# Optimization experiments

Hardware: AMD Instinct MI355X
Metric: run time of the kernel (lower is better)

## Reference

```python
import jax, jax.numpy as jnp
import numpy as np

B, DIM, HW = 2, 2, 512
HID, OUT, NL = 64, 3, 4  # no_layers=4 -> NL+1 filters


def _linear2d(w, b, inp):
    # 1x1 conv: w [o,i], inp [b,i,x,y] -> [b,o,x,y]
    return jnp.einsum('oi,bixy->boxy', w, inp) + b[None, :, None, None]


def _gabor_filter(x, w, b, mu_l, gamma_l, theta_l):
    # Rotated gaussian window. x: [B,2,H,W]
    ang = 2.0 * jnp.pi * theta_l  # [C]
    c, s = jnp.cos(ang), jnp.sin(ang)
    # rotation_matrix: rows [[cos, sin], [-sin, cos]] per channel -> [C,2,2]
    R = jnp.stack([jnp.stack([c, s], -1), jnp.stack([-s, c], -1)], -2)
    diff = x[:, None] - mu_l[None, :, :, None, None]          # [B,C,2,H,W]
    rot = jnp.einsum('coi,bcixy->bcoxy', R, diff)              # [B,C,2,H,W]
    g = jnp.exp(-0.5 * jnp.sum((gamma_l[None, :, :, None, None] * rot) ** 2, axis=2))
    return g * jnp.sin(_linear2d(w, b, x))                     # [B,C,H,W]


def setup_inputs() -> dict:
    key = jax.random.key(0)
    ks = jax.random.split(key, 10)
    inv_sqrt_hid = 1.0 / np.sqrt(HID)
    return {
        'x': jax.random.uniform(ks[0], (B, DIM, HW, HW), jnp.float32, -1.0, 1.0),
        'filt_w': jax.random.normal(ks[1], (NL + 1, HID, DIM), jnp.float32) * 0.1,
        'filt_b': jax.random.uniform(ks[2], (NL + 1, HID), jnp.float32, -np.pi, np.pi),
        'mu': jax.random.uniform(ks[3], (NL + 1, HID, DIM), jnp.float32, -1.0, 1.0),
        'gamma': jax.random.uniform(ks[4], (NL + 1, HID, DIM), jnp.float32, 0.5, 6.0),
        'theta': jax.random.uniform(ks[5], (NL + 1, HID), jnp.float32),
        'lin_w': jax.random.uniform(ks[6], (NL, HID, HID), jnp.float32, -inv_sqrt_hid, inv_sqrt_hid),
        'lin_b': jax.random.normal(ks[7], (NL, HID), jnp.float32) * 0.01,
        'out_w': jax.random.normal(ks[8], (OUT, HID), jnp.float32) * inv_sqrt_hid,
        'out_b': jax.random.normal(ks[9], (OUT,), jnp.float32) * 0.01,
    }


def reference(x, filt_w, filt_b, mu, gamma, theta, lin_w, lin_b, out_w, out_b):
    out = _gabor_filter(x, filt_w[0], filt_b[0], mu[0], gamma[0], theta[0])
    for i in range(1, NL + 1):
        lin = _linear2d(lin_w[i - 1], lin_b[i - 1], out)
        out = _gabor_filter(x, filt_w[i], filt_b[i], mu[i], gamma[i], theta[i]) * lin
    return _linear2d(out_w, out_b, out)  # [B,OUT,H,W]
```

## Files before the change

### kernel.cpp

```cpp
#include <hip/hip_runtime.h>
#include <hip/hip_bf16.h>
#include <math.h>

#define HW2 262144
#define TWO_PI     6.28318530717958647693f
#define INV_TWO_PI 0.15915494309189533577f
#define LOG2E      1.44269504088896340736f

typedef float  f32x4  __attribute__((ext_vector_type(4)));
typedef float  f32x8  __attribute__((ext_vector_type(8)));
typedef short  s16x8  __attribute__((ext_vector_type(8)));
typedef short  s16x4  __attribute__((ext_vector_type(4)));
typedef unsigned short ushort_t;

template <int I> struct ic { static constexpr int v = I; };
template <int I, int N, typename F>
__device__ __forceinline__ void sfor(F&& f) {
    if constexpr (I < N) { f(ic<I>{}); sfor<I + 1, N>(f); }
}

__device__ __forceinline__ ushort_t bf16_hi(float v) {
    __hip_bfloat16 h = __float2bfloat16(v);
    return __builtin_bit_cast(ushort_t, h);
}
__device__ __forceinline__ float bf16_tof(ushort_t u) {
    unsigned int x = ((unsigned int)u) << 16;
    return __builtin_bit_cast(float, x);
}

#define WS_WHI  15360
#define WS_WLO  48128
#define WS_WOH  80896
#define WS_WOL  82944

__global__ void gabor_pre(const float* __restrict__ filt_w,
                          const float* __restrict__ filt_b,
                          const float* __restrict__ mu,
                          const float* __restrict__ gamma,
                          const float* __restrict__ theta,
                          const float* __restrict__ lin_w,
                          const float* __restrict__ out_w,
                          float* __restrict__ pcq,
                          ushort_t* __restrict__ whi, ushort_t* __restrict__ wlo,
                          ushort_t* __restrict__ wouthi, ushort_t* __restrict__ woutlo) {
    int t = blockIdx.x * 256 + threadIdx.x;
    if (t < 320) {
        int i = t;
        float ang = TWO_PI * theta[i];
        float cs = cosf(ang), sn = sinf(ang);
        float g0 = gamma[i*2+0], g1 = gamma[i*2+1];
        float g0s = g0*g0, g1s = g1*g1;
        float cs2 = cs*cs, sn2 = sn*sn;
        float A = -0.5f * LOG2E * (g0s*cs2 + g1s*sn2);
        float B = -LOG2E * (cs*sn*(g0s - g1s));
        float C = -0.5f * LOG2E * (g0s*sn2 + g1s*cs2);
        float m0 = mu[i*2+0], m1 = mu[i*2+1];
        float* o = pcq + i*12;
        o[0] = A;  o[1] = B;  o[2] = C;
        o[3] = -(2.0f*A*m0 + B*m1);
        o[4] = -(B*m0 + 2.0f*C*m1);
        o[5] = A*m0*m0 + B*m0*m1 + C*m1*m1;
        o[6] = filt_w[i*2+0] * INV_TWO_PI;
        o[7] = filt_w[i*2+1] * INV_TWO_PI;
        o[8] = filt_b[i] * INV_TWO_PI;
        o[9] = 0.0f; o[10] = 0.0f; o[11] = 0.0f;
    } else if (t < 320 + 16384) {
        int i = t - 320;
        float w = lin_w[i];
        ushort_t h = bf16_hi(w);
        whi[i] = h;
        wlo[i] = bf16_hi(w - bf16_tof(h));
    } else if (t < 320 + 16384 + 1024) {
        int i = t - (320 + 16384);
        int m = i >> 6;
        float w = (m < 3) ? out_w[i] : 0.0f;
        ushort_t h = bf16_hi(w);
        wouthi[i] = h;
        woutlo[i] = bf16_hi(w - bf16_tof(h));
    }
}

__device__ __forceinline__ float geval(f32x4 qa, f32x4 qb, float br,
                                       float x0, float x1,
                                       float x02, float x11, float x12) {
    float t = fmaf(qa[0], x02, fmaf(qa[1], x11,
              fmaf(qa[2], x12, fmaf(qa[3], x0, fmaf(qb[0], x1, qb[1])))));
    float e  = __builtin_amdgcn_exp2f(t);
    float sa = fmaf(qb[2], x0, fmaf(qb[3], x1, br));
    return e * __builtin_amdgcn_sinf(sa);
}

__global__ __launch_bounds__(128, 2) void gabor_mfma(
    const float* __restrict__ x, const float* __restrict__ lin_b,
    const float* __restrict__ out_b, const float* __restrict__ pcq,
    const ushort_t* __restrict__ whi, const ushort_t* __restrict__ wlo,
    const ushort_t* __restrict__ wouthi, const ushort_t* __restrict__ woutlo,
    float* __restrict__ out) {
    __shared__ __attribute__((aligned(16))) unsigned char hbuf2[2][16384];
    const int lane = threadIdx.x & 63;
    const int wid  = threadIdx.x >> 6;
    const int g    = lane >> 4;
    const int lm   = lane & 15;
    const int base = blockIdx.x * 128 + wid * 64;
    unsigned char* hbuf = hbuf2[wid];

    f32x4 x0v, x1v, x02v, x11v, x12v;
    int pixo[4];
    sfor<0, 4>([&](auto NI) {
        int P  = base + NI.v*16 + lm;
        int bb = P >> 18, pix = P & (HW2 - 1);
        const float* xb = x + bb*(2*HW2) + pix;
        float a = xb[0], b = xb[HW2];
        x0v[NI.v] = a;  x1v[NI.v] = b;
        x02v[NI.v] = a*a;  x11v[NI.v] = a*b;  x12v[NI.v] = b*b;
        pixo[NI.v] = bb*(3*HW2) + pix;
    });

    sfor<0, 2>([&](auto KC) {
        f32x8 vv[4];
        sfor<0, 8>([&](auto J) {
            const float* q = pcq + (KC.v*32 + g*8 + J.v)*12;
            f32x4 qa = *(const f32x4*)q, qb = *(const f32x4*)(q + 4);
            float br = q[8];
            sfor<0, 4>([&](auto NI) {
                vv[NI.v][J.v] = geval(qa, qb, br, x0v[NI.v], x1v[NI.v],
                                      x02v[NI.v], x11v[NI.v], x12v[NI.v]);
            });
        });
        sfor<0, 4>([&](auto NI) {
            s16x8 fh, fl;
            sfor<0, 8>([&](auto J) {
                float v = vv[NI.v][J.v];
                ushort_t h = bf16_hi(v);
                fh[J.v] = (short)h;
                fl[J.v] = (short)bf16_hi(v - bf16_tof(h));
            });
            int px  = NI.v*16 + lm;
            int blk = (4*KC.v + g) ^ (px & 7);
            char* p0 = (char*)hbuf + px*128 + blk*16;
            *(s16x8*)(p0)        = fh;
            *(s16x8*)(p0 + 8192) = fl;
        });
    });

#pragma unroll 1
    for (int l = 1; l <= 4; ++l) {
        __syncthreads();
        const ushort_t* whl = whi + (l-1)*4096;
        const ushort_t* wll = wlo + (l-1)*4096;
        const float*    bv  = lin_b + (l-1)*64;
        f32x4 acc[4][4];
        sfor<0, 4>([&](auto MI) {
            f32x4 bias = *(const f32x4*)(bv + MI.v*16 + 4*g);
            sfor<0, 4>([&](auto NI) { acc[MI.v][NI.v] = bias; });
        });
        sfor<0, 2>([&](auto KC) {
            s16x8 bh[4], bl[4];
            sfor<0, 4>([&](auto NI) {
                int px  = NI.v*16 + lm;
                int blk = (4*KC.v + g) ^ (px & 7);
                const char* p0 = (const char*)hbuf + px*128 + blk*16;
                bh[NI.v] = *(const s16x8*)(p0);
                bl[NI.v] = *(const s16x8*)(p0 + 8192);
            });
            sfor<0, 4>([&](auto MI) {
                int off = (MI.v*16 + lm)*64 + KC.v*32 + g*8;
                s16x8 ah = *(const s16x8*)(whl + off);
                s16x8 al = *(const s16x8*)(wll + off);
                sfor<0, 4>([&](auto NI) {
                    f32x4 a = acc[MI.v][NI.v];
                    a = __builtin_amdgcn_mfma_f32_16x16x32_bf16(ah, bh[NI.v], a, 0, 0, 0);
                    a = __builtin_amdgcn_mfma_f32_16x16x32_bf16(ah, bl[NI.v], a, 0, 0, 0);
                    a = __builtin_amdgcn_mfma_f32_16x16x32_bf16(al, bh[NI.v], a, 0, 0, 0);
                    acc[MI.v][NI.v] = a;
                });
            });
        });
        __syncthreads();
        const float* pcl = pcq + l*768;
        sfor<0, 4>([&](auto MI) {
            f32x4 vo[4];
            sfor<0, 4>([&](auto R) {
                const float* q = pcl + (MI.v*16 + 4*g + R.v)*12;
                f32x4 qa = *(const f32x4*)q, qb = *(const f32x4*)(q + 4);
                float br = q[8];
                sfor<0, 4>([&](auto NI) {
                    vo[NI.v][R.v] = geval(qa, qb, br, x0v[NI.v], x1v[NI.v],
                                          x02v[NI.v], x11v[NI.v], x12v[NI.v])
                                    * acc[MI.v][NI.v][R.v];
                });
            });
            sfor<0, 4>([&](auto NI) {
                s16x4 fh, fl;
                sfor<0, 4>([&](auto R) {
                    float v = vo[NI.v][R.v];
                    ushort_t h = bf16_hi(v);
                    fh[R.v] = (short)h;
                    fl[R.v] = (short)bf16_hi(v - bf16_tof(h));
                });
                int px  = NI.v*16 + lm;
                int blk = (2*MI.v + (g >> 1)) ^ (px & 7);
                char* p0 = (char*)hbuf + px*128 + blk*16 + (g & 1)*8;
                *(s16x4*)(p0)        = fh;
                *(s16x4*)(p0 + 8192) = fl;
            });
        });
    }

    __syncthreads();
    f32x4 ao[4];
    sfor<0, 4>([&](auto NI) { ao[NI.v] = (f32x4)(0.0f); });
    sfor<0, 2>([&](auto KC) {
        s16x8 bh[4], bl[4];
        sfor<0, 4>([&](auto NI) {
            int px  = NI.v*16 + lm;
            int blk = (4*KC.v + g) ^ (px & 7);
            const char* p0 = (const char*)hbuf + px*128 + blk*16;
            bh[NI.v] = *(const s16x8*)(p0);
            bl[NI.v] = *(const s16x8*)(p0 + 8192);
        });
        int off = lm*64 + KC.v*32 + g*8;
        s16x8 ah = *(const s16x8*)(wouthi + off);
        s16x8 al = *(const s16x8*)(woutlo + off);
        sfor<0, 4>([&](auto NI) {
            f32x4 a = ao[NI.v];
            a = __builtin_amdgcn_mfma_f32_16x16x32_bf16(ah, bh[NI.v], a, 0, 0, 0);
            a = __builtin_amdgcn_mfma_f32_16x16x32_bf16(ah, bl[NI.v], a, 0, 0, 0);
            a = __builtin_amdgcn_mfma_f32_16x16x32_bf16(al, bh[NI.v], a, 0, 0, 0);
            ao[NI.v] = a;
        });
    });
    if (lane < 16) {
        float ob0 = out_b[0], ob1 = out_b[1], ob2 = out_b[2];
        sfor<0, 4>([&](auto NI) {
            float* po = out + pixo[NI.v];
            po[0]     = ao[NI.v][0] + ob0;
            po[HW2]   = ao[NI.v][1] + ob1;
            po[2*HW2] = ao[NI.v][2] + ob2;
        });
    }
}

extern "C" void kernel_launch(void* const* d_in, const int* in_sizes, int n_in,
                              void* d_out, int out_size, void* d_ws, size_t ws_size,
                              hipStream_t stream) {
    const float* x      = (const float*)d_in[0];
    const float* filt_w = (const float*)d_in[1];
    const float* filt_b = (const float*)d_in[2];
    const float* mu     = (const float*)d_in[3];
    const float* gamma  = (const float*)d_in[4];
    const float* theta  = (const float*)d_in[5];
    const float* lin_w  = (const float*)d_in[6];
    const float* lin_b  = (const float*)d_in[7];
    const float* out_w  = (const float*)d_in[8];
    const float* out_b  = (const float*)d_in[9];

    char* ws = (char*)d_ws;
    float*    pcq    = (float*)ws;
    ushort_t* whi    = (ushort_t*)(ws + WS_WHI);
    ushort_t* wlo    = (ushort_t*)(ws + WS_WLO);
    ushort_t* wouthi = (ushort_t*)(ws + WS_WOH);
    ushort_t* woutlo = (ushort_t*)(ws + WS_WOL);

    gabor_pre<<<70, 256, 0, stream>>>(filt_w, filt_b, mu, gamma, theta,
                                      lin_w, out_w, pcq, whi, wlo, wouthi, woutlo);
    gabor_mfma<<<4096, 128, 0, stream>>>(x, lin_b, out_b, pcq, whi, wlo,
                                         wouthi, woutlo, (float*)d_out);
}
```

Baseline: 158.2 us.

## Keep MFMA activations in registers via permuted K layout, dropping LDS round-trips

The lin and out weight columns are permuted in the preprocess kernel so that each MFMA accumulator output maps directly onto the B-operand fragment layout of the next layer. Activations can then stay in registers between layers, which removes the shared-memory staging buffer, the swizzled LDS stores and loads, and all __syncthreads. Block size goes from 128 to 256 threads with launch bounds (256,3). The cost is more live registers per thread (the bh/bl fragments for all pixel tiles), which may limit occupancy.

```diff
diff --git a/kernel.cpp b/kernel.cpp
--- a/kernel.cpp
+++ b/kernel.cpp
@@ -8,9 +8,7 @@
 #define LOG2E      1.44269504088896340736f
 
 typedef float  f32x4  __attribute__((ext_vector_type(4)));
-typedef float  f32x8  __attribute__((ext_vector_type(8)));
 typedef short  s16x8  __attribute__((ext_vector_type(8)));
-typedef short  s16x4  __attribute__((ext_vector_type(4)));
 typedef unsigned short ushort_t;
 
 template <int I> struct ic { static constexpr int v = I; };
@@ -26,6 +24,11 @@
 __device__ __forceinline__ float bf16_tof(ushort_t u) {
     unsigned int x = ((unsigned int)u) << 16;
     return __builtin_bit_cast(float, x);
+}
+
+__device__ __forceinline__ int kperm(int ks) {
+    int KC = ks >> 5, g = (ks >> 3) & 3, j = ks & 7;
+    return KC * 32 + (j >> 2) * 16 + g * 4 + (j & 3);
 }
 
 #define WS_WHI  15360
@@ -65,15 +68,16 @@
         o[8] = filt_b[i] * INV_TWO_PI;
         o[9] = 0.0f; o[10] = 0.0f; o[11] = 0.0f;
     } else if (t < 320 + 16384) {
-        int i = t - 320;
-        float w = lin_w[i];
+        int i  = t - 320;
+        int ks = i & 63;
+        float w = lin_w[(i - ks) + kperm(ks)];
         ushort_t h = bf16_hi(w);
         whi[i] = h;
         wlo[i] = bf16_hi(w - bf16_tof(h));
     } else if (t < 320 + 16384 + 1024) {
-        int i = t - (320 + 16384);
-        int m = i >> 6;
-        float w = (m < 3) ? out_w[i] : 0.0f;
+        int i  = t - (320 + 16384);
+        int m  = i >> 6, ks = i & 63;
+        float w = (m < 3) ? out_w[m*64 + kperm(ks)] : 0.0f;
         ushort_t h = bf16_hi(w);
         wouthi[i] = h;
         woutlo[i] = bf16_hi(w - bf16_tof(h));
@@ -90,19 +94,17 @@
     return e * __builtin_amdgcn_sinf(sa);
 }
 
-__global__ __launch_bounds__(128, 2) void gabor_mfma(
+__global__ __launch_bounds__(256, 3) void gabor_mfma(
     const float* __restrict__ x, const float* __restrict__ lin_b,
     const float* __restrict__ out_b, const float* __restrict__ pcq,
     const ushort_t* __restrict__ whi, const ushort_t* __restrict__ wlo,
     const ushort_t* __restrict__ wouthi, const ushort_t* __restrict__ woutlo,
     float* __restrict__ out) {
-    __shared__ __attribute__((aligned(16))) unsigned char hbuf2[2][16384];
     const int lane = threadIdx.x & 63;
     const int wid  = threadIdx.x >> 6;
     const int g    = lane >> 4;
     const int lm   = lane & 15;
-    const int base = blockIdx.x * 128 + wid * 64;
-    unsigned char* hbuf = hbuf2[wid];
+    const int base = blockIdx.x * 256 + wid * 64;
 
     f32x4 x0v, x1v, x02v, x11v, x12v;
     int pixo[4];
@@ -116,129 +118,91 @@
         pixo[NI.v] = bb*(3*HW2) + pix;
     });
 
-    sfor<0, 2>([&](auto KC) {
-        f32x8 vv[4];
-        sfor<0, 8>([&](auto J) {
-            const float* q = pcq + (KC.v*32 + g*8 + J.v)*12;
-            f32x4 qa = *(const f32x4*)q, qb = *(const f32x4*)(q + 4);
-            float br = q[8];
-            sfor<0, 4>([&](auto NI) {
-                vv[NI.v][J.v] = geval(qa, qb, br, x0v[NI.v], x1v[NI.v],
-                                      x02v[NI.v], x11v[NI.v], x12v[NI.v]);
-            });
-        });
-        sfor<0, 4>([&](auto NI) {
-            s16x8 fh, fl;
-            sfor<0, 8>([&](auto J) {
-                float v = vv[NI.v][J.v];
-                ushort_t h = bf16_hi(v);
-                fh[J.v] = (short)h;
-                fl[J.v] = (short)bf16_hi(v - bf16_tof(h));
-            });
-            int px  = NI.v*16 + lm;
-            int blk = (4*KC.v + g) ^ (px & 7);
-            char* p0 = (char*)hbuf + px*128 + blk*16;
-            *(s16x8*)(p0)        = fh;
-            *(s16x8*)(p0 + 8192) = fl;
-        });
+    s16x8 bh[4][2], bl[4][2];
+
+    auto mkfrag = [&](f32x4 vA, f32x4 vB, s16x8& fh, s16x8& fl) {
+        sfor<0, 4>([&](auto R) {
+            ushort_t hA = bf16_hi(vA[R.v]);
+            ushort_t hB = bf16_hi(vB[R.v]);
+            fh[R.v]     = (short)hA;
+            fh[R.v + 4] = (short)hB;
+            fl[R.v]     = (short)bf16_hi(vA[R.v] - bf16_tof(hA));
+            fl[R.v + 4] = (short)bf16_hi(vB[R.v] - bf16_tof(hB));
+        });
+    };
+
+    sfor<0, 4>([&](auto NI) {
+        f32x4 v[4];
+        sfor<0, 4>([&](auto MI) {
+            sfor<0, 4>([&](auto R) {
+                const float* q = pcq + (MI.v*16 + 4*g + R.v)*12;
+                f32x4 qa = *(const f32x4*)q, qb = *(const f32x4*)(q + 4);
+                v[MI.v][R.v] = geval(qa, qb, q[8], x0v[NI.v], x1v[NI.v],
+                                     x02v[NI.v], x11v[NI.v], x12v[NI.v]);
+            });
+        });
+        mkfrag(v[0], v[1], bh[NI.v][0], bl[NI.v][0]);
+        mkfrag(v[2], v[3], bh[NI.v][1], bl[NI.v][1]);
     });
 
 #pragma unroll 1
     for (int l = 1; l <= 4; ++l) {
-        __syncthreads();
         const ushort_t* whl = whi + (l-1)*4096;
         const ushort_t* wll = wlo + (l-1)*4096;
         const float*    bv  = lin_b + (l-1)*64;
-        f32x4 acc[4][4];
-        sfor<0, 4>([&](auto MI) {
-            f32x4 bias = *(const f32x4*)(bv + MI.v*16 + 4*g);
-            sfor<0, 4>([&](auto NI) { acc[MI.v][NI.v] = bias; });
-        });
+        const float*    pcl = pcq + l*768;
+        sfor<0, 4>([&](auto NI) {
+            constexpr int ni = NI.v;
+            f32x4 acc[4];
+            sfor<0, 4>([&](auto MI) {
+                acc[MI.v] = *(const f32x4*)(bv + MI.v*16 + 4*g);
+            });
+            sfor<0, 2>([&](auto KC) {
+                sfor<0, 4>([&](auto MI) {
+                    int off = (MI.v*16 + lm)*64 + KC.v*32 + g*8;
+                    s16x8 ah = *(const s16x8*)(whl + off);
+                    s16x8 al = *(const s16x8*)(wll + off);
+                    f32x4 a = acc[MI.v];
+                    a = __builtin_amdgcn_mfma_f32_16x16x32_bf16(ah, bh[ni][KC.v], a, 0, 0, 0);
+                    a = __builtin_amdgcn_mfma_f32_16x16x32_bf16(ah, bl[ni][KC.v], a, 0, 0, 0);
+                    a = __builtin_amdgcn_mfma_f32_16x16x32_bf16(al, bh[ni][KC.v], a, 0, 0, 0);
+                    acc[MI.v] = a;
+                });
+            });
+            f32x4 v[4];
+            sfor<0, 4>([&](auto MI) {
+                sfor<0, 4>([&](auto R) {
+                    const float* q = pcl + (MI.v*16 + 4*g + R.v)*12;
+                    f32x4 qa = *(const f32x4*)q, qb = *(const f32x4*)(q + 4);
+                    v[MI.v][R.v] = geval(qa, qb, q[8], x0v[ni], x1v[ni],
+                                         x02v[ni], x11v[ni], x12v[ni])
+                                   * acc[MI.v][R.v];
+                });
+            });
+            mkfrag(v[0], v[1], bh[ni][0], bl[ni][0]);
+            mkfrag(v[2], v[3], bh[ni][1], bl[ni][1]);
+        });
+    }
+
+    float ob0 = out_b[0], ob1 = out_b[1], ob2 = out_b[2];
+    sfor<0, 4>([&](auto NI) {
+        constexpr int ni = NI.v;
+        f32x4 ao = (f32x4)(0.0f);
         sfor<0, 2>([&](auto KC) {
-            s16x8 bh[4], bl[4];
-            sfor<0, 4>([&](auto NI) {
-                int px  = NI.v*16 + lm;
-                int blk = (4*KC.v + g) ^ (px & 7);
-                const char* p0 = (const char*)hbuf + px*128 + blk*16;
-                bh[NI.v] = *(const s16x8*)(p0);
-                bl[NI.v] = *(const s16x8*)(p0 + 8192);
-            });
-            sfor<0, 4>([&](auto MI) {
-                int off = (MI.v*16 + lm)*64 + KC.v*32 + g*8;
-                s16x8 ah = *(const s16x8*)(whl + off);
-                s16x8 al = *(const s16x8*)(wll + off);
-                sfor<0, 4>([&](auto NI) {
-                    f32x4 a = acc[MI.v][NI.v];
-                    a = __builtin_amdgcn_mfma_f32_16x16x32_bf16(ah, bh[NI.v], a, 0, 0, 0);
-                    a = __builtin_amdgcn_mfma_f32_16x16x32_bf16(ah, bl[NI.v], a, 0, 0, 0);
-                    a = __builtin_amdgcn_mfma_f32_16x16x32_bf16(al, bh[NI.v], a, 0, 0, 0);
-                    acc[MI.v][NI.v] = a;
-                });
-            });
-        });
-        __syncthreads();
-        const float* pcl = pcq + l*768;
-        sfor<0, 4>([&](auto MI) {
-            f32x4 vo[4];
-            sfor<0, 4>([&](auto R) {
-                const float* q = pcl + (MI.v*16 + 4*g + R.v)*12;
-                f32x4 qa = *(const f32x4*)q, qb = *(const f32x4*)(q + 4);
-                float br = q[8];
-                sfor<0, 4>([&](auto NI) {
-                    vo[NI.v][R.v] = geval(qa, qb, br, x0v[NI.v], x1v[NI.v],
-                                          x02v[NI.v], x11v[NI.v], x12v[NI.v])
-                                    * acc[MI.v][NI.v][R.v];
-                });
-            });
-            sfor<0, 4>([&](auto NI) {
-                s16x4 fh, fl;
-                sfor<0, 4>([&](auto R) {
-                    float v = vo[NI.v][R.v];
-                    ushort_t h = bf16_hi(v);
-                    fh[R.v] = (short)h;
-                    fl[R.v] = (short)bf16_hi(v - bf16_tof(h));
-                });
-                int px  = NI.v*16 + lm;
-                int blk = (2*MI.v + (g >> 1)) ^ (px & 7);
-                char* p0 = (char*)hbuf + px*128 + blk*16 + (g & 1)*8;
-                *(s16x4*)(p0)        = fh;
-                *(s16x4*)(p0 + 8192) = fl;
-            });
-        });
-    }
-
-    __syncthreads();
-    f32x4 ao[4];
-    sfor<0, 4>([&](auto NI) { ao[NI.v] = (f32x4)(0.0f); });
-    sfor<0, 2>([&](auto KC) {
-        s16x8 bh[4], bl[4];
-        sfor<0, 4>([&](auto NI) {
-            int px  = NI.v*16 + lm;
-            int blk = (4*KC.v + g) ^ (px & 7);
-            const char* p0 = (const char*)hbuf + px*128 + blk*16;
-            bh[NI.v] = *(const s16x8*)(p0);
-            bl[NI.v] = *(const s16x8*)(p0 + 8192);
-        });
-        int off = lm*64 + KC.v*32 + g*8;
-        s16x8 ah = *(const s16x8*)(wouthi + off);
-        s16x8 al = *(const s16x8*)(woutlo + off);
-        sfor<0, 4>([&](auto NI) {
-            f32x4 a = ao[NI.v];
-            a = __builtin_amdgcn_mfma_f32_16x16x32_bf16(ah, bh[NI.v], a, 0, 0, 0);
-            a = __builtin_amdgcn_mfma_f32_16x16x32_bf16(ah, bl[NI.v], a, 0, 0, 0);
-            a = __builtin_amdgcn_mfma_f32_16x16x32_bf16(al, bh[NI.v], a, 0, 0, 0);
-            ao[NI.v] = a;
-        });
+            int off = lm*64 + KC.v*32 + g*8;
+            s16x8 ah = *(const s16x8*)(wouthi + off);
+            s16x8 al = *(const s16x8*)(woutlo + off);
+            ao = __builtin_amdgcn_mfma_f32_16x16x32_bf16(ah, bh[ni][KC.v], ao, 0, 0, 0);
+            ao = __builtin_amdgcn_mfma_f32_16x16x32_bf16(ah, bl[ni][KC.v], ao, 0, 0, 0);
+            ao = __builtin_amdgcn_mfma_f32_16x16x32_bf16(al, bh[ni][KC.v], ao, 0, 0, 0);
+        });
+        if (lane < 16) {
+            float* po = out + pixo[ni];
+            po[0]     = ao[0] + ob0;
+            po[HW2]   = ao[1] + ob1;
+            po[2*HW2] = ao[2] + ob2;
+        }
     });
-    if (lane < 16) {
-        float ob0 = out_b[0], ob1 = out_b[1], ob2 = out_b[2];
-        sfor<0, 4>([&](auto NI) {
-            float* po = out + pixo[NI.v];
-            po[0]     = ao[NI.v][0] + ob0;
-            po[HW2]   = ao[NI.v][1] + ob1;
-            po[2*HW2] = ao[NI.v][2] + ob2;
-        });
-    }
 }
 
 extern "C" void kernel_launch(void* const* d_in, const int* in_sizes, int n_in,
@@ -264,6 +228,6 @@
 
     gabor_pre<<<70, 256, 0, stream>>>(filt_w, filt_b, mu, gamma, theta,
                                       lin_w, out_w, pcq, whi, wlo, wouthi, woutlo);
-    gabor_mfma<<<4096, 128, 0, stream>>>(x, lin_b, out_b, pcq, whi, wlo,
+    gabor_mfma<<<2048, 256, 0, stream>>>(x, lin_b, out_b, pcq, whi, wlo,
                                          wouthi, woutlo, (float*)d_out);
 }
```

Result: slower. 377.0 us (+138.3%).
